# Kernel optimization log

Hardware: AMD Instinct MI355X
Metric: run time of the kernel (lower is better)

Reference implementation:

```python
import jax, jax.numpy as jnp
import numpy as np

IN_DIM = 256
OUT_DIM = 64   # per-head dim
NUM_HEADS = 8
B = 8
N = 1024


def setup_inputs() -> dict:
    key = jax.random.key(0)
    k_adj, k_h, kq, kk, kv, kbq, kbk, kbv = jax.random.split(key, 8)
    adj_matrix = jax.random.randint(k_adj, (N, N), 0, 2, dtype=jnp.int32)
    h = jax.random.normal(k_h, (B, N, IN_DIM), dtype=jnp.float32)
    s = 1.0 / np.sqrt(IN_DIM)
    Wq = jax.random.normal(kq, (IN_DIM, OUT_DIM * NUM_HEADS), dtype=jnp.float32) * s
    Wk = jax.random.normal(kk, (IN_DIM, OUT_DIM * NUM_HEADS), dtype=jnp.float32) * s
    Wv = jax.random.normal(kv, (IN_DIM, OUT_DIM * NUM_HEADS), dtype=jnp.float32) * s
    bq = jax.random.normal(kbq, (OUT_DIM * NUM_HEADS,), dtype=jnp.float32) * 0.01
    bk = jax.random.normal(kbk, (OUT_DIM * NUM_HEADS,), dtype=jnp.float32) * 0.01
    bv = jax.random.normal(kbv, (OUT_DIM * NUM_HEADS,), dtype=jnp.float32) * 0.01
    return {"adj_matrix": adj_matrix, "h": h, "Wq": Wq, "bq": bq,
            "Wk": Wk, "bk": bk, "Wv": Wv, "bv": bv}


def reference(adj_matrix, h, Wq, bq, Wk, bk, Wv, bv):
    B_, N_, _ = h.shape
    H, D = NUM_HEADS, OUT_DIM
    Qh = (h @ Wq + bq).reshape(B_, N_, H, D)
    Kh = (h @ Wk + bk).reshape(B_, N_, H, D)
    Vh = (h @ Wv + bv).reshape(B_, N_, H, D)
    scores = jnp.einsum('bnhd,bmhd->bhnm', Qh, Kh) / jnp.sqrt(jnp.float32(D))
    # adjacency mask broadcast over batch and heads (neigh_attention=True)
    scores = jnp.where(adj_matrix[None, None, :, :] == 0, -jnp.inf, scores)
    attn = jax.nn.softmax(scores, axis=-1)
    out = jnp.einsum('bhnm,bmhd->bnhd', attn, Vh)
    return out.reshape(B_, N_, H * D)
```

## Files before the change

### kernel.cpp

```cpp
#include <hip/hip_runtime.h>
#include <hip/hip_bf16.h>
#include <math.h>

#define IN_DIM 256
#define HD     512
#define NHEADS 8
#define DH     64
#define NSEQ   1024
#define BATCH  8

#define QSCALE 0.18033688011112042f

typedef unsigned short u16;
typedef unsigned int   u32;
typedef short bf16x8 __attribute__((ext_vector_type(8)));
typedef float f32x4  __attribute__((ext_vector_type(4)));
typedef float f32x16 __attribute__((ext_vector_type(16)));

#if __has_builtin(__builtin_amdgcn_exp2f)
#define EXP2(x) __builtin_amdgcn_exp2f(x)
#else
#define EXP2(x) __expf(0.69314718056f * (x))
#endif

static __device__ __forceinline__ u16 f2bf(float x) {
    u32 u = __builtin_bit_cast(u32, x);
    u += 0x7FFFu + ((u >> 16) & 1u);
    return (u16)(u >> 16);
}
static __device__ __forceinline__ u32 pk(u16 a, u16 b) {
    return (u32)a | ((u32)b << 16);
}
static __device__ __forceinline__ u32 cvtpk(float a, float b) {
    __hip_bfloat162 t = __float22bfloat162_rn(make_float2(a, b));
    u32 r; __builtin_memcpy(&r, &t, 4);
    return r;
}
static __device__ __forceinline__ f32x16 maskinit(uint4 a, uint4 b) {
    f32x16 c;
    u32 ws[8] = {a.x, a.y, a.z, a.w, b.x, b.y, b.z, b.w};
#pragma unroll
    for (int i = 0; i < 8; ++i) {
        c[2 * i]     = __builtin_bit_cast(float, ws[i] << 16);
        c[2 * i + 1] = __builtin_bit_cast(float, ws[i] & 0xFFFF0000u);
    }
    return c;
}

__global__ __launch_bounds__(256)
void wtrans_kernel(const float* __restrict__ Wq, const float* __restrict__ Wk,
                   const float* __restrict__ Wv, u16* __restrict__ Wt)
{
    __shared__ float tile[64 * 65];
    const int bid = blockIdx.x, tid = threadIdx.x;
    const int k0 = (bid & 3) * 64, n0 = ((bid >> 2) & 7) * 64, wsel = bid >> 5;
    const float* W = (wsel == 0) ? Wq : (wsel == 1) ? Wk : Wv;
    u16* Out = Wt + (size_t)wsel * HD * IN_DIM;

    const int r = tid >> 2, c0 = (tid & 3) * 16;
#pragma unroll
    for (int j = 0; j < 16; j += 4) {
        float4 v = *(const float4*)(W + (size_t)(k0 + r) * HD + n0 + c0 + j);
        tile[r * 65 + c0 + j + 0] = v.x; tile[r * 65 + c0 + j + 1] = v.y;
        tile[r * 65 + c0 + j + 2] = v.z; tile[r * 65 + c0 + j + 3] = v.w;
    }
    __syncthreads();
    const int n = tid >> 2, ks = (tid & 3) * 16;
    u16 o[16];
#pragma unroll
    for (int j = 0; j < 16; ++j) o[j] = f2bf(tile[(ks + j) * 65 + n]);
    uint4 u0, u1;
    u0.x = pk(o[0], o[1]);   u0.y = pk(o[2], o[3]);
    u0.z = pk(o[4], o[5]);   u0.w = pk(o[6], o[7]);
    u1.x = pk(o[8], o[9]);   u1.y = pk(o[10], o[11]);
    u1.z = pk(o[12], o[13]); u1.w = pk(o[14], o[15]);
    u16* dst = Out + (size_t)(n0 + n) * IN_DIM + k0 + ks;
    *(uint4*)(dst) = u0;
    *(uint4*)(dst + 8) = u1;
}

__global__ __launch_bounds__(256, 4)
void gemm_mask_kernel(const float* __restrict__ h, const u16* __restrict__ Wt,
                      const int* __restrict__ adj,
                      const float* __restrict__ bq, const float* __restrict__ bk,
                      const float* __restrict__ bv,
                      u16* __restrict__ Qg, u16* __restrict__ Kg,
                      u16* __restrict__ Vtg, u16* __restrict__ Madd2)
{
    __shared__ u16 pool[64 * 64 + 3 * 64 * 64];
    const int tid = threadIdx.x;

    if (blockIdx.y >= 8) {
        int* tile = (int*)pool;
        const int abid = (blockIdx.y - 8) * 128 + blockIdx.x;
        const int tR = abid >> 4, tC = abid & 15;
        const int r = tid >> 2, cg = (tid & 3) * 16;
        const int* src = adj + (size_t)(tR * 64 + r) * NSEQ + tC * 64 + cg;
#pragma unroll
        for (int j = 0; j < 16; j += 4) {
            int4 a = *(const int4*)(src + j);
            tile[r * 65 + cg + j + 0] = a.x; tile[r * 65 + cg + j + 1] = a.y;
            tile[r * 65 + cg + j + 2] = a.z; tile[r * 65 + cg + j + 3] = a.w;
        }
        __syncthreads();
        const int q = tid >> 2, p0 = (tid & 3) * 16;
        u16 o[16];
#pragma unroll
        for (int j = 0; j < 16; ++j) {
            const int p = p0 + j;
            const int c = 32 * (p >> 5) + (p & 3) + 4 * ((p >> 4) & 1) + 8 * ((p >> 2) & 3);
            o[j] = (tile[q * 65 + c] == 0) ? (u16)0xFF7F : (u16)0;
        }
        uint4 u0, u1;
        u0.x = pk(o[0], o[1]);   u0.y = pk(o[2], o[3]);
        u0.z = pk(o[4], o[5]);   u0.w = pk(o[6], o[7]);
        u1.x = pk(o[8], o[9]);   u1.y = pk(o[10], o[11]);
        u1.z = pk(o[12], o[13]); u1.w = pk(o[14], o[15]);
        u16* dst = Madd2 + (size_t)(tR * 64 + q) * NSEQ + tC * 64 + p0;
        *(uint4*)(dst) = u0;
        *(uint4*)(dst + 8) = u1;
        return;
    }

    u16* As = pool;
    u16* Bs = pool + 64 * 64;

    const int m0 = blockIdx.x * 64;
    const int hh = blockIdx.y;
    const int n0 = hh * 64;

    const int w = tid >> 6, lane = tid & 63;
    const int l31 = lane & 31, half = lane >> 5;
    const int mh = w & 1, nh = w >> 1;
    const int s7 = l31 & 7;

    f32x16 acc[3] = {};

    const int arw = tid >> 2, acg = (tid & 3) * 2;
    const int brw = tid & 63, bgrp = tid >> 6;
    const float* srcA = h + (size_t)(m0 + arw) * IN_DIM;

    for (int kk = 0; kk < IN_DIM; kk += 64) {
        __syncthreads();
#pragma unroll
        for (int g = 0; g < 2; ++g) {
            const float* p = srcA + kk + (acg + g) * 8;
            float4 v0 = *(const float4*)(p);
            float4 v1 = *(const float4*)(p + 4);
            uint4 u;
            u.x = cvtpk(v0.x, v0.y); u.y = cvtpk(v0.z, v0.w);
            u.z = cvtpk(v1.x, v1.y); u.w = cvtpk(v1.z, v1.w);
            *(uint4*)&As[arw * 64 + (((acg + g) ^ (arw & 7)) * 8)] = u;
        }
#pragma unroll
        for (int i = 0; i < 6; ++i) {
            const int gc = bgrp * 6 + i;
            const int wh = gc >> 3, c8 = gc & 7;
            *(uint4*)&Bs[wh * 4096 + brw * 64 + ((c8 ^ (brw & 7)) * 8)] =
                *(const uint4*)(Wt + (size_t)wh * HD * IN_DIM +
                                (size_t)(n0 + brw) * IN_DIM + kk + c8 * 8);
        }
        __syncthreads();
        const int arow = (32 * mh + l31) * 64;
        const int brow = (32 * nh + l31) * 64;
#pragma unroll
        for (int s = 0; s < 4; ++s) {
            const int g = ((s * 2 + half) ^ s7) * 8;
            bf16x8 a = *(const bf16x8*)&As[arow + g];
#pragma unroll
            for (int wh = 0; wh < 3; ++wh) {
                bf16x8 b = *(const bf16x8*)&Bs[wh * 4096 + brow + g];
                acc[wh] = __builtin_amdgcn_mfma_f32_32x32x16_bf16(a, b, acc[wh], 0, 0, 0);
            }
        }
    }

    for (int which = 0; which < 2; ++which) {
        u16* T = pool;
        const float* bias = (which == 0) ? bq : bk;
        u16* Out = (which == 0) ? Qg : Kg;
        const float scale = (which == 0) ? QSCALE : 1.0f;
        const float bvv = bias[n0 + 32 * nh + l31];
        __syncthreads();
#pragma unroll
        for (int r = 0; r < 16; ++r) {
            const int row = 32 * mh + 4 * half + (r & 3) + 8 * (r >> 2);
            T[row * 72 + 32 * nh + l31] = f2bf((acc[which][r] + bvv) * scale);
        }
        __syncthreads();
        const int row = tid >> 2, qc = (tid & 3) * 16;
        u16* dst = Out + (size_t)(m0 + row) * HD + n0 + qc;
        const u16* srcT = &T[row * 72 + qc];
        *(uint4*)(dst)     = *(const uint4*)(srcT);
        *(uint4*)(dst + 8) = *(const uint4*)(srcT + 8);
    }

    {
        u16* T = pool;
        const int d = 32 * nh + l31;
        const float bvv = bv[n0 + d];
        __syncthreads();
#pragma unroll
        for (int g = 0; g < 4; ++g) {
            ushort4 o;
            o.x = f2bf(acc[2][4 * g + 0] + bvv);
            o.y = f2bf(acc[2][4 * g + 1] + bvv);
            o.z = f2bf(acc[2][4 * g + 2] + bvv);
            o.w = f2bf(acc[2][4 * g + 3] + bvv);
            *(ushort4*)&T[d * 72 + 32 * mh + 16 * half + 4 * g] = o;
        }
        __syncthreads();
        const int b = m0 >> 10, nloc = m0 & 1023;
        const int dd = tid >> 2, c = (tid & 3) * 16;
        u16* dst = Vtg + ((size_t)(b * NHEADS + hh) * DH + dd) * NSEQ + nloc + c;
        *(uint4*)(dst)     = *(uint4*)&T[dd * 72 + c];
        *(uint4*)(dst + 8) = *(uint4*)&T[dd * 72 + c + 8];
    }
}

__global__ __launch_bounds__(256, 2)
void attn_kernel(const u16* __restrict__ Madd2, const u16* __restrict__ Qg,
                 const u16* __restrict__ Kg, const u16* __restrict__ Vtg,
                 float* __restrict__ out)
{
    __shared__ u16 Ks[2][64 * 64];
    __shared__ u16 Vs[2][64 * 64];
    __shared__ u16 Ps[128 * 64];

    const int tid = threadIdx.x;
    const int w = tid >> 6, lane = tid & 63;
    const int l31 = lane & 31, half = lane >> 5;
    const int bh = blockIdx.x, qt = blockIdx.y;
    const int b = bh >> 3;
    const int n0 = qt * 128;
    const size_t rowbase = (size_t)b * NSEQ;
    const int colbase = (bh & 7) * DH;
    const int q7 = l31 & 7;
    const int qrow = w * 32 + l31;

    const u16* qg = Qg + (rowbase + n0 + qrow) * HD + colbase;
    bf16x8 qb[4];
#pragma unroll
    for (int s = 0; s < 4; ++s)
        qb[s] = *(const bf16x8*)(qg + s * 16 + half * 8);

    const int srow = tid >> 2, cp = (tid & 3) * 2;
    const int swc0 = ((cp ^ (srow & 7)) * 8), swc1 = (((cp + 1) ^ (srow & 7)) * 8);
    const u16* kgp = Kg + (rowbase + srow) * HD + colbase + cp * 8;
    const u16* vgp = Vtg + ((size_t)bh * DH + srow) * NSEQ + cp * 8;
    const u16* mrow = Madd2 + (size_t)(n0 + qrow) * NSEQ + half * 16;

    uint4 kG0 = *(const uint4*)kgp, kG1 = *(const uint4*)(kgp + 8);
    uint4 vG0 = *(const uint4*)vgp, vG1 = *(const uint4*)(vgp + 8);
    uint4 mA0 = *(const uint4*)(mrow);
    uint4 mB0 = *(const uint4*)(mrow + 8);
    uint4 mA1 = *(const uint4*)(mrow + 32);
    uint4 mB1 = *(const uint4*)(mrow + 40);

    *(uint4*)&Ks[0][srow * 64 + swc0] = kG0;
    *(uint4*)&Ks[0][srow * 64 + swc1] = kG1;
    *(uint4*)&Vs[0][srow * 64 + swc0] = vG0;
    *(uint4*)&Vs[0][srow * 64 + swc1] = vG1;
    __syncthreads();

    float lrow = 0.f;
    f32x16 O0 = {}, O1 = {};

    for (int ch = 0; ch < 16; ++ch) {
        const int cur = ch & 1;

        f32x16 st0 = maskinit(mA0, mB0);
        f32x16 st1 = maskinit(mA1, mB1);

        if (ch < 15) {
            kG0 = *(const uint4*)(kgp + (size_t)(ch + 1) * 64 * HD);
            kG1 = *(const uint4*)(kgp + (size_t)(ch + 1) * 64 * HD + 8);
            vG0 = *(const uint4*)(vgp + (ch + 1) * 64);
            vG1 = *(const uint4*)(vgp + (ch + 1) * 64 + 8);
            const u16* mnext = mrow + (ch + 1) * 64;
            mA0 = *(const uint4*)(mnext);
            mB0 = *(const uint4*)(mnext + 8);
            mA1 = *(const uint4*)(mnext + 32);
            mB1 = *(const uint4*)(mnext + 40);
        }

#pragma unroll
        for (int s = 0; s < 4; ++s) {
            const int g = ((s * 2 + half) ^ q7) * 8;
            bf16x8 ka0 = *(const bf16x8*)&Ks[cur][l31 * 64 + g];
            bf16x8 ka1 = *(const bf16x8*)&Ks[cur][(32 + l31) * 64 + g];
            st0 = __builtin_amdgcn_mfma_f32_32x32x16_bf16(ka0, qb[s], st0, 0, 0, 0);
            st1 = __builtin_amdgcn_mfma_f32_32x32x16_bf16(ka1, qb[s], st1, 0, 0, 0);
        }

        if (ch < 15) {
            *(uint4*)&Ks[1 - cur][srow * 64 + swc0] = kG0;
            *(uint4*)&Ks[1 - cur][srow * 64 + swc1] = kG1;
            *(uint4*)&Vs[1 - cur][srow * 64 + swc0] = vG0;
            *(uint4*)&Vs[1 - cur][srow * 64 + swc1] = vG1;
        }

#pragma unroll
        for (int tile = 0; tile < 2; ++tile) {
            const f32x16 st = tile ? st1 : st0;
            float p[16];
#pragma unroll
            for (int r = 0; r < 16; ++r) p[r] = EXP2(st[r]);
            float ps = 0.f;
#pragma unroll
            for (int r = 0; r < 16; ++r) ps += p[r];
            lrow += ps;
            uint4 w0, w1;
            w0.x = cvtpk(p[0], p[1]);   w0.y = cvtpk(p[2], p[3]);
            w0.z = cvtpk(p[4], p[5]);   w0.w = cvtpk(p[6], p[7]);
            w1.x = cvtpk(p[8], p[9]);   w1.y = cvtpk(p[10], p[11]);
            w1.z = cvtpk(p[12], p[13]); w1.w = cvtpk(p[14], p[15]);
            const int g = tile * 4 + half * 2;
            *(uint4*)&Ps[qrow * 64 + ((g ^ q7) * 8)]       = w0;
            *(uint4*)&Ps[qrow * 64 + (((g + 1) ^ q7) * 8)] = w1;
        }

#pragma unroll
        for (int s = 0; s < 4; ++s) {
            const int g = ((s * 2 + half) ^ q7) * 8;
            bf16x8 pb = *(const bf16x8*)&Ps[qrow * 64 + g];
            bf16x8 va0 = *(const bf16x8*)&Vs[cur][l31 * 64 + g];
            bf16x8 va1 = *(const bf16x8*)&Vs[cur][(32 + l31) * 64 + g];
            O0 = __builtin_amdgcn_mfma_f32_32x32x16_bf16(va0, pb, O0, 0, 0, 0);
            O1 = __builtin_amdgcn_mfma_f32_32x32x16_bf16(va1, pb, O1, 0, 0, 0);
        }
        __syncthreads();
    }

    lrow += __shfl_xor(lrow, 32, 64);
    const float inv = 1.0f / lrow;

    float* orow = out + (rowbase + n0 + qrow) * HD + colbase;
#pragma unroll
    for (int g = 0; g < 4; ++g) {
        const int d0 = 4 * half + 8 * g;
        float4 o0, o1;
        o0.x = O0[4 * g + 0] * inv; o0.y = O0[4 * g + 1] * inv;
        o0.z = O0[4 * g + 2] * inv; o0.w = O0[4 * g + 3] * inv;
        o1.x = O1[4 * g + 0] * inv; o1.y = O1[4 * g + 1] * inv;
        o1.z = O1[4 * g + 2] * inv; o1.w = O1[4 * g + 3] * inv;
        *(float4*)(orow + d0)      = o0;
        *(float4*)(orow + 32 + d0) = o1;
    }
}

extern "C" void kernel_launch(void* const* d_in, const int* in_sizes, int n_in,
                              void* d_out, int out_size, void* d_ws, size_t ws_size,
                              hipStream_t stream) {
    const int*   adj = (const int*)d_in[0];
    const float* h   = (const float*)d_in[1];
    const float* Wq  = (const float*)d_in[2];
    const float* bq  = (const float*)d_in[3];
    const float* Wk  = (const float*)d_in[4];
    const float* bk  = (const float*)d_in[5];
    const float* Wv  = (const float*)d_in[6];
    const float* bv  = (const float*)d_in[7];
    float* outp = (float*)d_out;

    u16* Wt    = (u16*)d_ws;
    u16* Qg    = Wt + (size_t)3 * HD * IN_DIM;
    u16* Kg    = Qg + (size_t)BATCH * NSEQ * HD;
    u16* Vtg   = Kg + (size_t)BATCH * NSEQ * HD;
    u16* Madd2 = Vtg + (size_t)BATCH * NSEQ * HD;

    wtrans_kernel<<<96, 256, 0, stream>>>(Wq, Wk, Wv, Wt);
    gemm_mask_kernel<<<dim3(BATCH * NSEQ / 64, 10), 256, 0, stream>>>(
        h, Wt, adj, bq, bk, bv, Qg, Kg, Vtg, Madd2);
    attn_kernel<<<dim3(BATCH * NHEADS, NSEQ / 128), 256, 0, stream>>>(
        Madd2, Qg, Kg, Vtg, outp);
}
```

Measured before the change: 131.3 us.

## Double query rows per wave, keep P in registers via permlane swap

Each wave now handles 64 query rows (two 32-row tiles) instead of 32, so each K/V tile read from shared memory is reused across twice as many queries. The grid shrinks to 256 query rows per block. The P matrix no longer goes through shared memory: the bf16 probabilities are rearranged across lanes with permlane32_swap (or a shuffle fallback) and fed straight into the PV MFMA. K/V global prefetch now runs two chunks ahead with ping-pong register sets. The cost is higher register pressure, occupancy hint cut to 1 block per CU, and half as many blocks (256), which risks underfilling the GPU.

```diff
diff --git a/kernel.cpp b/kernel.cpp
--- a/kernel.cpp
+++ b/kernel.cpp
@@ -16,6 +16,7 @@
 typedef short bf16x8 __attribute__((ext_vector_type(8)));
 typedef float f32x4  __attribute__((ext_vector_type(4)));
 typedef float f32x16 __attribute__((ext_vector_type(16)));
+typedef unsigned int u32x2 __attribute__((ext_vector_type(2)));
 
 #if __has_builtin(__builtin_amdgcn_exp2f)
 #define EXP2(x) __builtin_amdgcn_exp2f(x)
@@ -45,6 +46,51 @@
         c[2 * i + 1] = __builtin_bit_cast(float, ws[i] & 0xFFFF0000u);
     }
     return c;
+}
+
+static __device__ __forceinline__ void pswap(u32 &a, u32 &b) {
+#if __has_builtin(__builtin_amdgcn_permlane32_swap)
+    u32x2 r = __builtin_amdgcn_permlane32_swap(a, b, false, false);
+    a = r.x; b = r.y;
+#else
+    const bool hi = (threadIdx.x & 32) != 0;
+    u32 as = (u32)__shfl_xor((int)a, 32, 64);
+    u32 bs = (u32)__shfl_xor((int)b, 32, 64);
+    u32 na = hi ? bs : a;
+    u32 nb = hi ? b  : as;
+    a = na; b = nb;
+#endif
+}
+
+#define MFMA32(a, b, c) __builtin_amdgcn_mfma_f32_32x32x16_bf16(a, b, c, 0, 0, 0)
+
+static __device__ __forceinline__ float sm_pack(const f32x16 s0, const f32x16 s1,
+                                                bf16x8* pb) {
+    float p0[16], p1[16];
+#pragma unroll
+    for (int r = 0; r < 16; ++r) p0[r] = EXP2(s0[r]);
+#pragma unroll
+    for (int r = 0; r < 16; ++r) p1[r] = EXP2(s1[r]);
+    float t0 = (((p0[0] + p0[1]) + (p0[2] + p0[3])) + ((p0[4] + p0[5]) + (p0[6] + p0[7])))
+             + (((p0[8] + p0[9]) + (p0[10] + p0[11])) + ((p0[12] + p0[13]) + (p0[14] + p0[15])));
+    float t1 = (((p1[0] + p1[1]) + (p1[2] + p1[3])) + ((p1[4] + p1[5]) + (p1[6] + p1[7])))
+             + (((p1[8] + p1[9]) + (p1[10] + p1[11])) + ((p1[12] + p1[13]) + (p1[14] + p1[15])));
+    uint4 w0, w1, w2, w3;
+    w0.x = cvtpk(p0[0], p0[1]);   w0.y = cvtpk(p0[2], p0[3]);
+    w0.z = cvtpk(p0[4], p0[5]);   w0.w = cvtpk(p0[6], p0[7]);
+    w1.x = cvtpk(p0[8], p0[9]);   w1.y = cvtpk(p0[10], p0[11]);
+    w1.z = cvtpk(p0[12], p0[13]); w1.w = cvtpk(p0[14], p0[15]);
+    w2.x = cvtpk(p1[0], p1[1]);   w2.y = cvtpk(p1[2], p1[3]);
+    w2.z = cvtpk(p1[4], p1[5]);   w2.w = cvtpk(p1[6], p1[7]);
+    w3.x = cvtpk(p1[8], p1[9]);   w3.y = cvtpk(p1[10], p1[11]);
+    w3.z = cvtpk(p1[12], p1[13]); w3.w = cvtpk(p1[14], p1[15]);
+    pswap(w0.x, w1.x); pswap(w0.y, w1.y); pswap(w0.z, w1.z); pswap(w0.w, w1.w);
+    pswap(w2.x, w3.x); pswap(w2.y, w3.y); pswap(w2.z, w3.z); pswap(w2.w, w3.w);
+    pb[0] = __builtin_bit_cast(bf16x8, w0);
+    pb[1] = __builtin_bit_cast(bf16x8, w1);
+    pb[2] = __builtin_bit_cast(bf16x8, w2);
+    pb[3] = __builtin_bit_cast(bf16x8, w3);
+    return t0 + t1;
 }
 
 __global__ __launch_bounds__(256)
@@ -218,134 +264,151 @@
     }
 }
 
-__global__ __launch_bounds__(256, 2)
+__global__ __launch_bounds__(256, 1)
 void attn_kernel(const u16* __restrict__ Madd2, const u16* __restrict__ Qg,
                  const u16* __restrict__ Kg, const u16* __restrict__ Vtg,
                  float* __restrict__ out)
 {
     __shared__ u16 Ks[2][64 * 64];
     __shared__ u16 Vs[2][64 * 64];
-    __shared__ u16 Ps[128 * 64];
 
     const int tid = threadIdx.x;
     const int w = tid >> 6, lane = tid & 63;
     const int l31 = lane & 31, half = lane >> 5;
     const int bh = blockIdx.x, qt = blockIdx.y;
     const int b = bh >> 3;
-    const int n0 = qt * 128;
+    const int n0 = qt * 256;
     const size_t rowbase = (size_t)b * NSEQ;
     const int colbase = (bh & 7) * DH;
     const int q7 = l31 & 7;
-    const int qrow = w * 32 + l31;
-
-    const u16* qg = Qg + (rowbase + n0 + qrow) * HD + colbase;
-    bf16x8 qb[4];
-#pragma unroll
-    for (int s = 0; s < 4; ++s)
-        qb[s] = *(const bf16x8*)(qg + s * 16 + half * 8);
+    const int qA = w * 64 + l31;
+    const int qB = qA + 32;
+
+    const u16* qga = Qg + (rowbase + n0 + qA) * HD + colbase;
+    const u16* qgb = Qg + (rowbase + n0 + qB) * HD + colbase;
+    bf16x8 qbA[4], qbB[4];
+#pragma unroll
+    for (int s = 0; s < 4; ++s) {
+        qbA[s] = *(const bf16x8*)(qga + s * 16 + half * 8);
+        qbB[s] = *(const bf16x8*)(qgb + s * 16 + half * 8);
+    }
 
     const int srow = tid >> 2, cp = (tid & 3) * 2;
     const int swc0 = ((cp ^ (srow & 7)) * 8), swc1 = (((cp + 1) ^ (srow & 7)) * 8);
     const u16* kgp = Kg + (rowbase + srow) * HD + colbase + cp * 8;
     const u16* vgp = Vtg + ((size_t)bh * DH + srow) * NSEQ + cp * 8;
-    const u16* mrow = Madd2 + (size_t)(n0 + qrow) * NSEQ + half * 16;
-
-    uint4 kG0 = *(const uint4*)kgp, kG1 = *(const uint4*)(kgp + 8);
-    uint4 vG0 = *(const uint4*)vgp, vG1 = *(const uint4*)(vgp + 8);
-    uint4 mA0 = *(const uint4*)(mrow);
-    uint4 mB0 = *(const uint4*)(mrow + 8);
-    uint4 mA1 = *(const uint4*)(mrow + 32);
-    uint4 mB1 = *(const uint4*)(mrow + 40);
-
-    *(uint4*)&Ks[0][srow * 64 + swc0] = kG0;
-    *(uint4*)&Ks[0][srow * 64 + swc1] = kG1;
-    *(uint4*)&Vs[0][srow * 64 + swc0] = vG0;
-    *(uint4*)&Vs[0][srow * 64 + swc1] = vG1;
+    const u16* mrowA = Madd2 + (size_t)(n0 + qA) * NSEQ + half * 16;
+    const u16* mrowB = Madd2 + (size_t)(n0 + qB) * NSEQ + half * 16;
+
+    uint4 mA0a = *(const uint4*)(mrowA);
+    uint4 mA0b = *(const uint4*)(mrowA + 8);
+    uint4 mA1a = *(const uint4*)(mrowA + 32);
+    uint4 mA1b = *(const uint4*)(mrowA + 40);
+    uint4 mB0a = *(const uint4*)(mrowB);
+    uint4 mB0b = *(const uint4*)(mrowB + 8);
+    uint4 mB1a = *(const uint4*)(mrowB + 32);
+    uint4 mB1b = *(const uint4*)(mrowB + 40);
+
+    uint4 s0k0, s0k1, s0v0, s0v1;
+    uint4 s1k0, s1k1, s1v0, s1v1;
+    s0k0 = *(const uint4*)kgp;       s0k1 = *(const uint4*)(kgp + 8);
+    s0v0 = *(const uint4*)vgp;       s0v1 = *(const uint4*)(vgp + 8);
+    *(uint4*)&Ks[0][srow * 64 + swc0] = s0k0;
+    *(uint4*)&Ks[0][srow * 64 + swc1] = s0k1;
+    *(uint4*)&Vs[0][srow * 64 + swc0] = s0v0;
+    *(uint4*)&Vs[0][srow * 64 + swc1] = s0v1;
+    s1k0 = *(const uint4*)(kgp + (size_t)64 * HD);
+    s1k1 = *(const uint4*)(kgp + (size_t)64 * HD + 8);
+    s1v0 = *(const uint4*)(vgp + 64);
+    s1v1 = *(const uint4*)(vgp + 64 + 8);
     __syncthreads();
 
-    float lrow = 0.f;
-    f32x16 O0 = {}, O1 = {};
-
-    for (int ch = 0; ch < 16; ++ch) {
-        const int cur = ch & 1;
-
-        f32x16 st0 = maskinit(mA0, mB0);
-        f32x16 st1 = maskinit(mA1, mB1);
-
-        if (ch < 15) {
-            kG0 = *(const uint4*)(kgp + (size_t)(ch + 1) * 64 * HD);
-            kG1 = *(const uint4*)(kgp + (size_t)(ch + 1) * 64 * HD + 8);
-            vG0 = *(const uint4*)(vgp + (ch + 1) * 64);
-            vG1 = *(const uint4*)(vgp + (ch + 1) * 64 + 8);
-            const u16* mnext = mrow + (ch + 1) * 64;
-            mA0 = *(const uint4*)(mnext);
-            mB0 = *(const uint4*)(mnext + 8);
-            mA1 = *(const uint4*)(mnext + 32);
-            mB1 = *(const uint4*)(mnext + 40);
-        }
-
-#pragma unroll
-        for (int s = 0; s < 4; ++s) {
-            const int g = ((s * 2 + half) ^ q7) * 8;
-            bf16x8 ka0 = *(const bf16x8*)&Ks[cur][l31 * 64 + g];
-            bf16x8 ka1 = *(const bf16x8*)&Ks[cur][(32 + l31) * 64 + g];
-            st0 = __builtin_amdgcn_mfma_f32_32x32x16_bf16(ka0, qb[s], st0, 0, 0, 0);
-            st1 = __builtin_amdgcn_mfma_f32_32x32x16_bf16(ka1, qb[s], st1, 0, 0, 0);
-        }
-
-        if (ch < 15) {
-            *(uint4*)&Ks[1 - cur][srow * 64 + swc0] = kG0;
-            *(uint4*)&Ks[1 - cur][srow * 64 + swc1] = kG1;
-            *(uint4*)&Vs[1 - cur][srow * 64 + swc0] = vG0;
-            *(uint4*)&Vs[1 - cur][srow * 64 + swc1] = vG1;
-        }
-
-#pragma unroll
-        for (int tile = 0; tile < 2; ++tile) {
-            const f32x16 st = tile ? st1 : st0;
-            float p[16];
-#pragma unroll
-            for (int r = 0; r < 16; ++r) p[r] = EXP2(st[r]);
-            float ps = 0.f;
-#pragma unroll
-            for (int r = 0; r < 16; ++r) ps += p[r];
-            lrow += ps;
-            uint4 w0, w1;
-            w0.x = cvtpk(p[0], p[1]);   w0.y = cvtpk(p[2], p[3]);
-            w0.z = cvtpk(p[4], p[5]);   w0.w = cvtpk(p[6], p[7]);
-            w1.x = cvtpk(p[8], p[9]);   w1.y = cvtpk(p[10], p[11]);
-            w1.z = cvtpk(p[12], p[13]); w1.w = cvtpk(p[14], p[15]);
-            const int g = tile * 4 + half * 2;
-            *(uint4*)&Ps[qrow * 64 + ((g ^ q7) * 8)]       = w0;
-            *(uint4*)&Ps[qrow * 64 + (((g + 1) ^ q7) * 8)] = w1;
-        }
-
-#pragma unroll
-        for (int s = 0; s < 4; ++s) {
-            const int g = ((s * 2 + half) ^ q7) * 8;
-            bf16x8 pb = *(const bf16x8*)&Ps[qrow * 64 + g];
-            bf16x8 va0 = *(const bf16x8*)&Vs[cur][l31 * 64 + g];
-            bf16x8 va1 = *(const bf16x8*)&Vs[cur][(32 + l31) * 64 + g];
-            O0 = __builtin_amdgcn_mfma_f32_32x32x16_bf16(va0, pb, O0, 0, 0, 0);
-            O1 = __builtin_amdgcn_mfma_f32_32x32x16_bf16(va1, pb, O1, 0, 0, 0);
-        }
-        __syncthreads();
-    }
-
-    lrow += __shfl_xor(lrow, 32, 64);
-    const float inv = 1.0f / lrow;
-
-    float* orow = out + (rowbase + n0 + qrow) * HD + colbase;
+    float lA = 0.f, lB = 0.f;
+    f32x16 OA0 = {}, OA1 = {}, OB0 = {}, OB1 = {};
+
+#define CHUNK(CH, CUR, KW, KL)                                                 \
+    {                                                                          \
+        f32x16 sA0 = maskinit(mA0a, mA0b);                                     \
+        f32x16 sA1 = maskinit(mA1a, mA1b);                                     \
+        f32x16 sB0 = maskinit(mB0a, mB0b);                                     \
+        f32x16 sB1 = maskinit(mB1a, mB1b);                                     \
+        if ((CH) < 15) {                                                       \
+            const u16* ma = mrowA + ((CH) + 1) * 64;                           \
+            const u16* mb = mrowB + ((CH) + 1) * 64;                           \
+            mA0a = *(const uint4*)(ma);      mA0b = *(const uint4*)(ma + 8);   \
+            mA1a = *(const uint4*)(ma + 32); mA1b = *(const uint4*)(ma + 40);  \
+            mB0a = *(const uint4*)(mb);      mB0b = *(const uint4*)(mb + 8);   \
+            mB1a = *(const uint4*)(mb + 32); mB1b = *(const uint4*)(mb + 40);  \
+        }                                                                      \
+        _Pragma("unroll")                                                      \
+        for (int s = 0; s < 4; ++s) {                                          \
+            const int g = ((s * 2 + half) ^ q7) * 8;                           \
+            bf16x8 ka0 = *(const bf16x8*)&Ks[CUR][l31 * 64 + g];               \
+            bf16x8 ka1 = *(const bf16x8*)&Ks[CUR][(32 + l31) * 64 + g];        \
+            sA0 = MFMA32(ka0, qbA[s], sA0);                                    \
+            sA1 = MFMA32(ka1, qbA[s], sA1);                                    \
+            sB0 = MFMA32(ka0, qbB[s], sB0);                                    \
+            sB1 = MFMA32(ka1, qbB[s], sB1);                                    \
+        }                                                                      \
+        if ((CH) < 15) {                                                       \
+            *(uint4*)&Ks[1 - (CUR)][srow * 64 + swc0] = KW##k0;                \
+            *(uint4*)&Ks[1 - (CUR)][srow * 64 + swc1] = KW##k1;                \
+            *(uint4*)&Vs[1 - (CUR)][srow * 64 + swc0] = KW##v0;                \
+            *(uint4*)&Vs[1 - (CUR)][srow * 64 + swc1] = KW##v1;                \
+        }                                                                      \
+        if ((CH) < 14) {                                                       \
+            const size_t ko = (size_t)((CH) + 2) * 64 * HD;                    \
+            const int    vo = ((CH) + 2) * 64;                                 \
+            KL##k0 = *(const uint4*)(kgp + ko);                                \
+            KL##k1 = *(const uint4*)(kgp + ko + 8);                            \
+            KL##v0 = *(const uint4*)(vgp + vo);                                \
+            KL##v1 = *(const uint4*)(vgp + vo + 8);                            \
+        }                                                                      \
+        bf16x8 pbA[4], pbB[4];                                                 \
+        lA += sm_pack(sA0, sA1, pbA);                                          \
+        lB += sm_pack(sB0, sB1, pbB);                                          \
+        _Pragma("unroll")                                                      \
+        for (int s = 0; s < 4; ++s) {                                          \
+            const int g = ((s * 2 + half) ^ q7) * 8;                           \
+            bf16x8 va0 = *(const bf16x8*)&Vs[CUR][l31 * 64 + g];               \
+            bf16x8 va1 = *(const bf16x8*)&Vs[CUR][(32 + l31) * 64 + g];        \
+            OA0 = MFMA32(va0, pbA[s], OA0);                                    \
+            OA1 = MFMA32(va1, pbA[s], OA1);                                    \
+            OB0 = MFMA32(va0, pbB[s], OB0);                                    \
+            OB1 = MFMA32(va1, pbB[s], OB1);                                    \
+        }                                                                      \
+        __syncthreads();                                                       \
+    }
+
+    for (int ch = 0; ch < 16; ch += 2) {
+        CHUNK(ch,     0, s1, s0)
+        CHUNK(ch + 1, 1, s0, s1)
+    }
+#undef CHUNK
+
+    lA += __shfl_xor(lA, 32, 64);
+    lB += __shfl_xor(lB, 32, 64);
+    const float invA = 1.0f / lA;
+    const float invB = 1.0f / lB;
+
+    float* orowA = out + (rowbase + n0 + qA) * HD + colbase;
+    float* orowB = out + (rowbase + n0 + qB) * HD + colbase;
 #pragma unroll
     for (int g = 0; g < 4; ++g) {
         const int d0 = 4 * half + 8 * g;
-        float4 o0, o1;
-        o0.x = O0[4 * g + 0] * inv; o0.y = O0[4 * g + 1] * inv;
-        o0.z = O0[4 * g + 2] * inv; o0.w = O0[4 * g + 3] * inv;
-        o1.x = O1[4 * g + 0] * inv; o1.y = O1[4 * g + 1] * inv;
-        o1.z = O1[4 * g + 2] * inv; o1.w = O1[4 * g + 3] * inv;
-        *(float4*)(orow + d0)      = o0;
-        *(float4*)(orow + 32 + d0) = o1;
+        float4 a0, a1, b0, b1;
+        a0.x = OA0[4 * g + 0] * invA; a0.y = OA0[4 * g + 1] * invA;
+        a0.z = OA0[4 * g + 2] * invA; a0.w = OA0[4 * g + 3] * invA;
+        a1.x = OA1[4 * g + 0] * invA; a1.y = OA1[4 * g + 1] * invA;
+        a1.z = OA1[4 * g + 2] * invA; a1.w = OA1[4 * g + 3] * invA;
+        b0.x = OB0[4 * g + 0] * invB; b0.y = OB0[4 * g + 1] * invB;
+        b0.z = OB0[4 * g + 2] * invB; b0.w = OB0[4 * g + 3] * invB;
+        b1.x = OB1[4 * g + 0] * invB; b1.y = OB1[4 * g + 1] * invB;
+        b1.z = OB1[4 * g + 2] * invB; b1.w = OB1[4 * g + 3] * invB;
+        *(float4*)(orowA + d0)      = a0;
+        *(float4*)(orowA + 32 + d0) = a1;
+        *(float4*)(orowB + d0)      = b0;
+        *(float4*)(orowB + 32 + d0) = b1;
     }
 }
 
@@ -367,10 +430,11 @@
     u16* Kg    = Qg + (size_t)BATCH * NSEQ * HD;
     u16* Vtg   = Kg + (size_t)BATCH * NSEQ * HD;
     u16* Madd2 = Vtg + (size_t)BATCH * NSEQ * HD;
+    (void)ws_size;
 
     wtrans_kernel<<<96, 256, 0, stream>>>(Wq, Wk, Wv, Wt);
     gemm_mask_kernel<<<dim3(BATCH * NSEQ / 64, 10), 256, 0, stream>>>(
         h, Wt, adj, bq, bk, bv, Qg, Kg, Vtg, Madd2);
-    attn_kernel<<<dim3(BATCH * NHEADS, NSEQ / 128), 256, 0, stream>>>(
+    attn_kernel<<<dim3(BATCH * NHEADS, NSEQ / 256), 256, 0, stream>>>(
         Madd2, Qg, Kg, Vtg, outp);
 }
```

Result: slower. 136.0 us (+3.5%).

## Split attention key range across two wave teams with async LDS loads and register P

Applied to the files above, without the earlier changes.

The attention kernel moves to 512 threads, with two teams of four waves each handling half of the key chunks (split-K). Their partial O and row sums are merged through shared memory at the end. K/V tiles are now staged with global_load_lds direct-to-LDS copies. The softmax P tile stays in registers via permlane32 swaps instead of round-tripping through an LDS Ps buffer, and score computation is split into halves interleaved with PV MFMAs. This aims to raise wave-level parallelism and cut LDS traffic, at the cost of a final reduction and higher register and occupancy demands.

```diff
diff --git a/kernel.cpp b/kernel.cpp
--- a/kernel.cpp
+++ b/kernel.cpp
@@ -16,6 +16,7 @@
 typedef short bf16x8 __attribute__((ext_vector_type(8)));
 typedef float f32x4  __attribute__((ext_vector_type(4)));
 typedef float f32x16 __attribute__((ext_vector_type(16)));
+typedef unsigned int u32x2 __attribute__((ext_vector_type(2)));
 
 #if __has_builtin(__builtin_amdgcn_exp2f)
 #define EXP2(x) __builtin_amdgcn_exp2f(x)
@@ -45,6 +46,44 @@
         c[2 * i + 1] = __builtin_bit_cast(float, ws[i] & 0xFFFF0000u);
     }
     return c;
+}
+
+static __device__ __forceinline__ void pswap(u32 &a, u32 &b) {
+#if __has_builtin(__builtin_amdgcn_permlane32_swap)
+    u32x2 r = __builtin_amdgcn_permlane32_swap(a, b, false, false);
+    a = r.x; b = r.y;
+#else
+    const bool hi = (threadIdx.x & 32) != 0;
+    u32 as = (u32)__shfl_xor((int)a, 32, 64);
+    u32 bs = (u32)__shfl_xor((int)b, 32, 64);
+    u32 na = hi ? bs : a;
+    u32 nb = hi ? b  : as;
+    a = na; b = nb;
+#endif
+}
+
+#define MFMA32(a, b, c) __builtin_amdgcn_mfma_f32_32x32x16_bf16(a, b, c, 0, 0, 0)
+
+#define GLOAD16(G, L)                                                          \
+    __builtin_amdgcn_global_load_lds(                                          \
+        (const __attribute__((address_space(1))) unsigned int*)(const void*)(G),\
+        (__attribute__((address_space(3))) unsigned int*)(void*)(L), 16, 0, 0)
+
+static __device__ __forceinline__ float sm_pack_half(const f32x16 st, bf16x8* pb) {
+    float p[16];
+#pragma unroll
+    for (int r = 0; r < 16; ++r) p[r] = EXP2(st[r]);
+    float t = (((p[0] + p[1]) + (p[2] + p[3])) + ((p[4] + p[5]) + (p[6] + p[7])))
+            + (((p[8] + p[9]) + (p[10] + p[11])) + ((p[12] + p[13]) + (p[14] + p[15])));
+    uint4 w0, w1;
+    w0.x = cvtpk(p[0], p[1]);   w0.y = cvtpk(p[2], p[3]);
+    w0.z = cvtpk(p[4], p[5]);   w0.w = cvtpk(p[6], p[7]);
+    w1.x = cvtpk(p[8], p[9]);   w1.y = cvtpk(p[10], p[11]);
+    w1.z = cvtpk(p[12], p[13]); w1.w = cvtpk(p[14], p[15]);
+    pswap(w0.x, w1.x); pswap(w0.y, w1.y); pswap(w0.z, w1.z); pswap(w0.w, w1.w);
+    pb[0] = __builtin_bit_cast(bf16x8, w0);
+    pb[1] = __builtin_bit_cast(bf16x8, w1);
+    return t;
 }
 
 __global__ __launch_bounds__(256)
@@ -218,17 +257,17 @@
     }
 }
 
-__global__ __launch_bounds__(256, 2)
+__global__ __launch_bounds__(512, 4)
 void attn_kernel(const u16* __restrict__ Madd2, const u16* __restrict__ Qg,
                  const u16* __restrict__ Kg, const u16* __restrict__ Vtg,
                  float* __restrict__ out)
 {
-    __shared__ u16 Ks[2][64 * 64];
-    __shared__ u16 Vs[2][64 * 64];
-    __shared__ u16 Ps[128 * 64];
+    __shared__ __align__(16) u16 Ks[2][2][4096];
+    __shared__ __align__(16) u16 Vs[2][2][4096];
 
     const int tid = threadIdx.x;
     const int w = tid >> 6, lane = tid & 63;
+    const int team = w >> 2, j = w & 3;
     const int l31 = lane & 31, half = lane >> 5;
     const int bh = blockIdx.x, qt = blockIdx.y;
     const int b = bh >> 3;
@@ -236,116 +275,138 @@
     const size_t rowbase = (size_t)b * NSEQ;
     const int colbase = (bh & 7) * DH;
     const int q7 = l31 & 7;
-    const int qrow = w * 32 + l31;
-
-    const u16* qg = Qg + (rowbase + n0 + qrow) * HD + colbase;
+    const int qA = j * 32 + l31;
+    const int cbase = team * 8;
+
+    const u16* qga = Qg + (rowbase + n0 + qA) * HD + colbase;
     bf16x8 qb[4];
 #pragma unroll
     for (int s = 0; s < 4; ++s)
-        qb[s] = *(const bf16x8*)(qg + s * 16 + half * 8);
-
-    const int srow = tid >> 2, cp = (tid & 3) * 2;
-    const int swc0 = ((cp ^ (srow & 7)) * 8), swc1 = (((cp + 1) ^ (srow & 7)) * 8);
-    const u16* kgp = Kg + (rowbase + srow) * HD + colbase + cp * 8;
-    const u16* vgp = Vtg + ((size_t)bh * DH + srow) * NSEQ + cp * 8;
-    const u16* mrow = Madd2 + (size_t)(n0 + qrow) * NSEQ + half * 16;
-
-    uint4 kG0 = *(const uint4*)kgp, kG1 = *(const uint4*)(kgp + 8);
-    uint4 vG0 = *(const uint4*)vgp, vG1 = *(const uint4*)(vgp + 8);
-    uint4 mA0 = *(const uint4*)(mrow);
-    uint4 mB0 = *(const uint4*)(mrow + 8);
-    uint4 mA1 = *(const uint4*)(mrow + 32);
-    uint4 mB1 = *(const uint4*)(mrow + 40);
-
-    *(uint4*)&Ks[0][srow * 64 + swc0] = kG0;
-    *(uint4*)&Ks[0][srow * 64 + swc1] = kG1;
-    *(uint4*)&Vs[0][srow * 64 + swc0] = vG0;
-    *(uint4*)&Vs[0][srow * 64 + swc1] = vG1;
+        qb[s] = *(const bf16x8*)(qga + s * 16 + half * 8);
+
+    const int lrow = lane >> 3, lgran = (lane & 7) ^ lrow;
+    const int br0 = j * 16, br1 = j * 16 + 8;
+    const u16* kg0 = Kg + (rowbase + cbase * 64 + br0 + lrow) * HD + colbase + lgran * 8;
+    const u16* kg1 = kg0 + (size_t)8 * HD;
+    const u16* vg0 = Vtg + ((size_t)bh * DH + br0 + lrow) * NSEQ + cbase * 64 + lgran * 8;
+    const u16* vg1 = vg0 + (size_t)8 * NSEQ;
+
+#define STAGE(BUF, CH)                                                   \
+    do {                                                                 \
+        GLOAD16(kg0 + (size_t)(CH) * 64 * HD, &Ks[team][BUF][br0 * 64]); \
+        GLOAD16(kg1 + (size_t)(CH) * 64 * HD, &Ks[team][BUF][br1 * 64]); \
+        GLOAD16(vg0 + (CH) * 64,              &Vs[team][BUF][br0 * 64]); \
+        GLOAD16(vg1 + (CH) * 64,              &Vs[team][BUF][br1 * 64]); \
+    } while (0)
+
+    const u16* mrow = Madd2 + (size_t)(n0 + qA) * NSEQ + cbase * 64 + half * 16;
+
+    STAGE(0, 0);
+    uint4 m0a = *(const uint4*)(mrow);
+    uint4 m0b = *(const uint4*)(mrow + 8);
+    uint4 m1a = *(const uint4*)(mrow + 32);
+    uint4 m1b = *(const uint4*)(mrow + 40);
     __syncthreads();
 
-    float lrow = 0.f;
+    float l = 0.f;
     f32x16 O0 = {}, O1 = {};
 
-    for (int ch = 0; ch < 16; ++ch) {
+    for (int ch = 0; ch < 8; ++ch) {
         const int cur = ch & 1;
-
-        f32x16 st0 = maskinit(mA0, mB0);
-        f32x16 st1 = maskinit(mA1, mB1);
-
-        if (ch < 15) {
-            kG0 = *(const uint4*)(kgp + (size_t)(ch + 1) * 64 * HD);
-            kG1 = *(const uint4*)(kgp + (size_t)(ch + 1) * 64 * HD + 8);
-            vG0 = *(const uint4*)(vgp + (ch + 1) * 64);
-            vG1 = *(const uint4*)(vgp + (ch + 1) * 64 + 8);
-            const u16* mnext = mrow + (ch + 1) * 64;
-            mA0 = *(const uint4*)(mnext);
-            mB0 = *(const uint4*)(mnext + 8);
-            mA1 = *(const uint4*)(mnext + 32);
-            mB1 = *(const uint4*)(mnext + 40);
-        }
-
+        const u16* Kc = &Ks[team][cur][0];
+        const u16* Vc = &Vs[team][cur][0];
+
+        if (ch < 7) STAGE(1 - cur, ch + 1);
+
+        f32x16 s0 = maskinit(m0a, m0b);
 #pragma unroll
         for (int s = 0; s < 4; ++s) {
             const int g = ((s * 2 + half) ^ q7) * 8;
-            bf16x8 ka0 = *(const bf16x8*)&Ks[cur][l31 * 64 + g];
-            bf16x8 ka1 = *(const bf16x8*)&Ks[cur][(32 + l31) * 64 + g];
-            st0 = __builtin_amdgcn_mfma_f32_32x32x16_bf16(ka0, qb[s], st0, 0, 0, 0);
-            st1 = __builtin_amdgcn_mfma_f32_32x32x16_bf16(ka1, qb[s], st1, 0, 0, 0);
-        }
-
-        if (ch < 15) {
-            *(uint4*)&Ks[1 - cur][srow * 64 + swc0] = kG0;
-            *(uint4*)&Ks[1 - cur][srow * 64 + swc1] = kG1;
-            *(uint4*)&Vs[1 - cur][srow * 64 + swc0] = vG0;
-            *(uint4*)&Vs[1 - cur][srow * 64 + swc1] = vG1;
-        }
-
-#pragma unroll
-        for (int tile = 0; tile < 2; ++tile) {
-            const f32x16 st = tile ? st1 : st0;
-            float p[16];
-#pragma unroll
-            for (int r = 0; r < 16; ++r) p[r] = EXP2(st[r]);
-            float ps = 0.f;
-#pragma unroll
-            for (int r = 0; r < 16; ++r) ps += p[r];
-            lrow += ps;
-            uint4 w0, w1;
-            w0.x = cvtpk(p[0], p[1]);   w0.y = cvtpk(p[2], p[3]);
-            w0.z = cvtpk(p[4], p[5]);   w0.w = cvtpk(p[6], p[7]);
-            w1.x = cvtpk(p[8], p[9]);   w1.y = cvtpk(p[10], p[11]);
-            w1.z = cvtpk(p[12], p[13]); w1.w = cvtpk(p[14], p[15]);
-            const int g = tile * 4 + half * 2;
-            *(uint4*)&Ps[qrow * 64 + ((g ^ q7) * 8)]       = w0;
-            *(uint4*)&Ps[qrow * 64 + (((g + 1) ^ q7) * 8)] = w1;
-        }
-
+            bf16x8 ka = *(const bf16x8*)&Kc[l31 * 64 + g];
+            s0 = MFMA32(ka, qb[s], s0);
+        }
+        bf16x8 pb[2];
+        l += sm_pack_half(s0, pb);
+
+#pragma unroll
+        for (int s = 0; s < 2; ++s) {
+            const int g = ((s * 2 + half) ^ q7) * 8;
+            bf16x8 va0 = *(const bf16x8*)&Vc[l31 * 64 + g];
+            bf16x8 va1 = *(const bf16x8*)&Vc[(32 + l31) * 64 + g];
+            O0 = MFMA32(va0, pb[s], O0);
+            O1 = MFMA32(va1, pb[s], O1);
+        }
+
+        f32x16 s1 = maskinit(m1a, m1b);
+        if (ch < 7) {
+            const u16* mn = mrow + (ch + 1) * 64;
+            m0a = *(const uint4*)(mn);      m0b = *(const uint4*)(mn + 8);
+            m1a = *(const uint4*)(mn + 32); m1b = *(const uint4*)(mn + 40);
+        }
 #pragma unroll
         for (int s = 0; s < 4; ++s) {
             const int g = ((s * 2 + half) ^ q7) * 8;
-            bf16x8 pb = *(const bf16x8*)&Ps[qrow * 64 + g];
-            bf16x8 va0 = *(const bf16x8*)&Vs[cur][l31 * 64 + g];
-            bf16x8 va1 = *(const bf16x8*)&Vs[cur][(32 + l31) * 64 + g];
-            O0 = __builtin_amdgcn_mfma_f32_32x32x16_bf16(va0, pb, O0, 0, 0, 0);
-            O1 = __builtin_amdgcn_mfma_f32_32x32x16_bf16(va1, pb, O1, 0, 0, 0);
-        }
-        __syncthreads();
-    }
-
-    lrow += __shfl_xor(lrow, 32, 64);
-    const float inv = 1.0f / lrow;
-
-    float* orow = out + (rowbase + n0 + qrow) * HD + colbase;
-#pragma unroll
-    for (int g = 0; g < 4; ++g) {
-        const int d0 = 4 * half + 8 * g;
-        float4 o0, o1;
-        o0.x = O0[4 * g + 0] * inv; o0.y = O0[4 * g + 1] * inv;
-        o0.z = O0[4 * g + 2] * inv; o0.w = O0[4 * g + 3] * inv;
-        o1.x = O1[4 * g + 0] * inv; o1.y = O1[4 * g + 1] * inv;
-        o1.z = O1[4 * g + 2] * inv; o1.w = O1[4 * g + 3] * inv;
-        *(float4*)(orow + d0)      = o0;
-        *(float4*)(orow + 32 + d0) = o1;
+            bf16x8 ka = *(const bf16x8*)&Kc[(32 + l31) * 64 + g];
+            s1 = MFMA32(ka, qb[s], s1);
+        }
+        l += sm_pack_half(s1, pb);
+
+#pragma unroll
+        for (int s = 2; s < 4; ++s) {
+            const int g = ((s * 2 + half) ^ q7) * 8;
+            bf16x8 va0 = *(const bf16x8*)&Vc[l31 * 64 + g];
+            bf16x8 va1 = *(const bf16x8*)&Vc[(32 + l31) * 64 + g];
+            O0 = MFMA32(va0, pb[s - 2], O0);
+            O1 = MFMA32(va1, pb[s - 2], O1);
+        }
+        __syncthreads();
+    }
+#undef STAGE
+
+    float4* Oex = (float4*)&Ks[0][0][0];
+    float*  Lex = (float*)&Vs[0][0][0];
+
+    if (team == 1) {
+#pragma unroll
+        for (int g = 0; g < 4; ++g) {
+            float4 t;
+            t.x = O0[4 * g + 0]; t.y = O0[4 * g + 1];
+            t.z = O0[4 * g + 2]; t.w = O0[4 * g + 3];
+            Oex[(j * 8 + g) * 64 + lane] = t;
+            t.x = O1[4 * g + 0]; t.y = O1[4 * g + 1];
+            t.z = O1[4 * g + 2]; t.w = O1[4 * g + 3];
+            Oex[(j * 8 + 4 + g) * 64 + lane] = t;
+        }
+        Lex[j * 64 + lane] = l;
+    }
+    __syncthreads();
+    if (team == 0) {
+        l += Lex[j * 64 + lane];
+#pragma unroll
+        for (int g = 0; g < 4; ++g) {
+            float4 t0 = Oex[(j * 8 + g) * 64 + lane];
+            float4 t1 = Oex[(j * 8 + 4 + g) * 64 + lane];
+            O0[4 * g + 0] += t0.x; O0[4 * g + 1] += t0.y;
+            O0[4 * g + 2] += t0.z; O0[4 * g + 3] += t0.w;
+            O1[4 * g + 0] += t1.x; O1[4 * g + 1] += t1.y;
+            O1[4 * g + 2] += t1.z; O1[4 * g + 3] += t1.w;
+        }
+
+        l += __shfl_xor(l, 32, 64);
+        const float inv = 1.0f / l;
+
+        float* orow = out + (rowbase + n0 + qA) * HD + colbase;
+#pragma unroll
+        for (int g = 0; g < 4; ++g) {
+            const int d0 = 4 * half + 8 * g;
+            float4 a0, a1;
+            a0.x = O0[4 * g + 0] * inv; a0.y = O0[4 * g + 1] * inv;
+            a0.z = O0[4 * g + 2] * inv; a0.w = O0[4 * g + 3] * inv;
+            a1.x = O1[4 * g + 0] * inv; a1.y = O1[4 * g + 1] * inv;
+            a1.z = O1[4 * g + 2] * inv; a1.w = O1[4 * g + 3] * inv;
+            *(float4*)(orow + d0)      = a0;
+            *(float4*)(orow + 32 + d0) = a1;
+        }
     }
 }
 
@@ -367,10 +428,11 @@
     u16* Kg    = Qg + (size_t)BATCH * NSEQ * HD;
     u16* Vtg   = Kg + (size_t)BATCH * NSEQ * HD;
     u16* Madd2 = Vtg + (size_t)BATCH * NSEQ * HD;
+    (void)ws_size;
 
     wtrans_kernel<<<96, 256, 0, stream>>>(Wq, Wk, Wv, Wt);
     gemm_mask_kernel<<<dim3(BATCH * NSEQ / 64, 10), 256, 0, stream>>>(
         h, Wt, adj, bq, bk, bv, Qg, Kg, Vtg, Madd2);
-    attn_kernel<<<dim3(BATCH * NHEADS, NSEQ / 128), 256, 0, stream>>>(
+    attn_kernel<<<dim3(BATCH * NHEADS, NSEQ / 128), 512, 0, stream>>>(
         Madd2, Qg, Kg, Vtg, outp);
 }
```

Result: no change. 132.1 us (+0.6%).
